# Performance work log

Measured on AMD Instinct MI355X. Metric: run time of the kernel, lower is better.

Reference implementation:

```python
import jax, jax.numpy as jnp
import numpy as np

B, T, H = 8, 4096, 512
K = 8192  # codebook size


def setup_inputs() -> dict:
    key = jax.random.key(0)
    kz, ke = jax.random.split(key)
    z = jax.random.normal(kz, (B, T, H), dtype=jnp.float32)
    emb = jax.random.normal(ke, (K, H), dtype=jnp.float32) * 0.02
    return {"z": z, "emb": emb}


def reference(z, emb):
    b, t, h = z.shape
    flat = z.reshape(b * t, h)
    dist = (jnp.sum(flat * flat, axis=1, keepdims=True)
            - 2.0 * (flat @ emb.T)
            + jnp.sum(emb * emb, axis=1)[None, :])
    idx = jnp.argmin(dist, axis=1)            # (b*t,)
    z_q = emb[idx].reshape(b, t, h)           # codebook lookup
    # straight-through estimator
    z_st = z + jax.lax.stop_gradient(z_q - z)
    codebook_loss = jnp.mean((z_q - jax.lax.stop_gradient(z)) ** 2)
    commit_loss = jnp.mean((z - jax.lax.stop_gradient(z_q)) ** 2)
    return z_st, idx.reshape(b, t), codebook_loss, commit_loss
```

## Files before the change

### kernel.cpp

```cpp
#include <hip/hip_runtime.h>
#include <cstdint>
#include <cstddef>

#define M_ROWS 32768
#define K_CODES 8192
#define H_DIM 512
#define TAU 2.5e-4f
#define MAXFLAG 32768

typedef float  f32x4 __attribute__((ext_vector_type(4)));
typedef short  s16x8 __attribute__((ext_vector_type(8)));

typedef __attribute__((address_space(3))) void as3_void;
typedef const __attribute__((address_space(1))) void as1_cvoid;
#define GLD16(gp, lp) __builtin_amdgcn_global_load_lds((as1_cvoid*)(gp), (as3_void*)(lp), 16, 0, 0)

__device__ __forceinline__ unsigned short f2bf(float f) {
    uint32_t u = __float_as_uint(f);
    u = u + 0x7fffu + ((u >> 16) & 1u);
    return (unsigned short)(u >> 16);
}
__device__ __forceinline__ float bf2f(unsigned short h) {
    return __uint_as_float(((uint32_t)h) << 16);
}

__global__ __launch_bounds__(256) void split_all_kernel(
    const float* __restrict__ z, const float* __restrict__ emb,
    unsigned short* __restrict__ zh, unsigned short* __restrict__ zl,
    unsigned short* __restrict__ eh, unsigned short* __restrict__ el)
{
    const int ZQ = M_ROWS * H_DIM / 4;
    const int EQ = K_CODES * H_DIM / 4;
    int t = blockIdx.x * 256 + threadIdx.x;
    const float* src; unsigned short* hi; unsigned short* lo;
    if (t < ZQ)           { src = z;   hi = zh; lo = zl; }
    else if (t < ZQ + EQ) { t -= ZQ; src = emb; hi = eh; lo = el; }
    else return;
    const float4 v = reinterpret_cast<const float4*>(src)[t];
    ushort4 h, l;
    h.x = f2bf(v.x); l.x = f2bf(v.x - bf2f(h.x));
    h.y = f2bf(v.y); l.y = f2bf(v.y - bf2f(h.y));
    h.z = f2bf(v.z); l.z = f2bf(v.z - bf2f(h.z));
    h.w = f2bf(v.w); l.w = f2bf(v.w - bf2f(h.w));
    reinterpret_cast<ushort4*>(hi)[t] = h;
    reinterpret_cast<ushort4*>(lo)[t] = l;
}

__device__ __forceinline__ float np_sumsq_row32(const float* __restrict__ row,
                                                int lane32) {
    const int c = lane32 >> 3, j = lane32 & 7;
    const float* p = row + c * 128 + j;
    float s = __fmul_rn(p[0], p[0]);
    #pragma unroll
    for (int t = 1; t < 16; ++t) {
        const float v = p[8 * t];
        s = __fadd_rn(s, __fmul_rn(v, v));
    }
    s = __fadd_rn(s, __shfl_xor(s, 1));
    s = __fadd_rn(s, __shfl_xor(s, 2));
    s = __fadd_rn(s, __shfl_xor(s, 4));
    s = __fadd_rn(s, __shfl_xor(s, 8));
    s = __fadd_rn(s, __shfl_xor(s, 16));
    return s;
}

__global__ __launch_bounds__(256) void rowsq_all_kernel(
    const float* __restrict__ z, const float* __restrict__ emb,
    float* __restrict__ x2, float* __restrict__ e2,
    float* __restrict__ loss_slots, int* __restrict__ flag_count)
{
    const int slot = blockIdx.x * 8 + (threadIdx.x >> 5);
    if (slot < M_ROWS) {
        const float s = np_sumsq_row32(z + (size_t)slot * H_DIM, threadIdx.x & 31);
        if ((threadIdx.x & 31) == 0) x2[slot] = s;
    } else if (slot < M_ROWS + K_CODES) {
        const int r = slot - M_ROWS;
        const float s = np_sumsq_row32(emb + (size_t)r * H_DIM, threadIdx.x & 31);
        if ((threadIdx.x & 31) == 0) e2[r] = s;
    }
    if (blockIdx.x == 0) {
        if (threadIdx.x < 2) loss_slots[threadIdx.x] = 0.f;
        if (threadIdx.x == 0) *flag_count = 0;
    }
}

__device__ __forceinline__ void top2_merge(float& b1, int& ix, float& b2,
                                           float ob1, int oix, float ob2) {
    if (ob1 < b1)      { b2 = fminf(b1, ob2); b1 = ob1; ix = oix; }
    else if (ob1 > b1) { b2 = fminf(b2, ob1); }
    else               { if (oix < ix) ix = oix; b2 = b1; }
}

__global__ __launch_bounds__(512, 1) void mfma_dist_kernel(
    const unsigned short* __restrict__ zh, const unsigned short* __restrict__ zl,
    const unsigned short* __restrict__ eh, const unsigned short* __restrict__ el,
    const float* __restrict__ x2, const float* __restrict__ e2,
    float* __restrict__ pb1, float* __restrict__ pb2, int* __restrict__ pidx)
{
    __shared__ __align__(16) unsigned short lb[2][4][8192];

    const int tid = threadIdx.x;
    const int l   = tid & 63;
    const int w   = tid >> 6;
    const int wm  = w >> 2;
    const int wn  = w & 3;

    const int bid  = blockIdx.x;
    const int xcd  = bid & 7;
    const int sq   = bid >> 3;
    const int band = sq >> 7;
    const int r128 = sq & 127;
    const int ct   = r128 >> 2;
    const int rt   = (band * 8 + xcd) * 4 + (r128 & 3);
    const int row0 = rt * 256;
    const int c0   = ct * 256;

    const int m    = w >> 1;
    const int half = w & 1;
    const unsigned short* sp = (m == 0) ? zh : (m == 1) ? zl : (m == 2) ? eh : el;
    const int rbase0 = (m < 2) ? row0 : c0;
    const unsigned short* sb = sp
        + (size_t)(rbase0 + half * 128 + (l >> 2)) * H_DIM
        + ((l & 3) ^ ((l >> 3) & 3)) * 8;

    const int aoff = (wm * 128 + (l & 15)) * 64 + (((l >> 4) ^ ((l >> 1) & 3)) * 16);
    const int boff = (wn * 64  + (l & 15)) * 64 + (((l >> 4) ^ ((l >> 1) & 3)) * 16);

    f32x4 acc[8][4];
    #pragma unroll
    for (int i = 0; i < 8; ++i)
        #pragma unroll
        for (int j = 0; j < 4; ++j)
            acc[i][j] = (f32x4){0.f, 0.f, 0.f, 0.f};

    {
        char* dst = (char*)&lb[0][m][0] + half * 8192;
        #pragma unroll
        for (int t = 0; t < 8; ++t)
            GLD16(sb + (size_t)t * 16 * H_DIM, dst + t * 1024);
    }
    asm volatile("s_waitcnt vmcnt(0)" ::: "memory");
    __builtin_amdgcn_s_barrier();

    for (int s = 0; s < 16; ++s) {
        const int par = s & 1;

        if (s < 15) {
            const unsigned short* src = sb + (s + 1) * 32;
            char* dst = (char*)&lb[par ^ 1][m][0] + half * 8192;
            #pragma unroll
            for (int t = 0; t < 8; ++t)
                GLD16(src + (size_t)t * 16 * H_DIM, dst + t * 1024);
            asm volatile("s_waitcnt vmcnt(8)" ::: "memory");
        } else {
            asm volatile("s_waitcnt vmcnt(0)" ::: "memory");
        }
        __builtin_amdgcn_s_barrier();

        const char* pAh = (const char*)&lb[par][0][0];
        const char* pAl = (const char*)&lb[par][1][0];
        const char* pBh = (const char*)&lb[par][2][0];
        const char* pBl = (const char*)&lb[par][3][0];

        s16x8 ah[8];
        #pragma unroll
        for (int i = 0; i < 8; ++i)
            ah[i] = *(const s16x8*)(pAh + aoff + i * 1024);
        s16x8 bh[4], bv[4];
        #pragma unroll
        for (int j = 0; j < 4; ++j) {
            bh[j] = *(const s16x8*)(pBh + boff + j * 1024);
            bv[j] = *(const s16x8*)(pBl + boff + j * 1024);
        }

        __builtin_amdgcn_s_setprio(1);
        #pragma unroll
        for (int j = 0; j < 4; ++j)
            #pragma unroll
            for (int i = 0; i < 8; ++i)
                acc[i][j] = __builtin_amdgcn_mfma_f32_16x16x32_bf16(ah[i], bv[j], acc[i][j], 0, 0, 0);
        s16x8 avA[4];
        #pragma unroll
        for (int i = 0; i < 4; ++i)
            avA[i] = *(const s16x8*)(pAl + aoff + i * 1024);
        #pragma unroll
        for (int j = 0; j < 4; ++j)
            #pragma unroll
            for (int i = 0; i < 8; ++i)
                acc[i][j] = __builtin_amdgcn_mfma_f32_16x16x32_bf16(ah[i], bh[j], acc[i][j], 0, 0, 0);
        s16x8 avB[4];
        #pragma unroll
        for (int i = 0; i < 4; ++i)
            avB[i] = *(const s16x8*)(pAl + aoff + (4 + i) * 1024);
        #pragma unroll
        for (int j = 0; j < 4; ++j)
            #pragma unroll
            for (int i = 0; i < 4; ++i)
                acc[i][j] = __builtin_amdgcn_mfma_f32_16x16x32_bf16(avA[i], bh[j], acc[i][j], 0, 0, 0);
        #pragma unroll
        for (int j = 0; j < 4; ++j)
            #pragma unroll
            for (int i = 0; i < 4; ++i)
                acc[4 + i][j] = __builtin_amdgcn_mfma_f32_16x16x32_bf16(avB[i], bh[j], acc[4 + i][j], 0, 0, 0);
        __builtin_amdgcn_s_setprio(0);

        __builtin_amdgcn_s_barrier();
    }

    float* mb1 = (float*)&lb[0][0][0];
    float* mb2 = mb1 + 1024;
    int*   mi  = (int*)(mb1 + 2048);

    float e2v[4];
    #pragma unroll
    for (int j = 0; j < 4; ++j)
        e2v[j] = e2[c0 + wn * 64 + j * 16 + (l & 15)];

    #pragma unroll
    for (int i = 0; i < 8; ++i) {
        const float4 x2v = *reinterpret_cast<const float4*>(
            x2 + row0 + wm * 128 + i * 16 + (l >> 4) * 4);
        const float x2a[4] = {x2v.x, x2v.y, x2v.z, x2v.w};
        #pragma unroll
        for (int r = 0; r < 4; ++r) {
            float b1 = 3.4e38f, b2 = 3.4e38f; int ix = 0;
            #pragma unroll
            for (int j = 0; j < 4; ++j) {
                const float d = __fadd_rn(__fmaf_rn(-2.f, acc[i][j][r], x2a[r]), e2v[j]);
                const int cj = c0 + wn * 64 + j * 16 + (l & 15);
                if (d < b1)      { b2 = b1; b1 = d; ix = cj; }
                else if (d < b2) { b2 = d; }
            }
            #pragma unroll
            for (int mm = 1; mm <= 8; mm <<= 1) {
                const float ob1 = __shfl_xor(b1, mm);
                const float ob2 = __shfl_xor(b2, mm);
                const int   oix = __shfl_xor(ix, mm);
                top2_merge(b1, ix, b2, ob1, oix, ob2);
            }
            if ((l & 15) == 0) {
                const int rl = wm * 128 + i * 16 + (l >> 4) * 4 + r;
                mb1[wn * 256 + rl] = b1;
                mb2[wn * 256 + rl] = b2;
                mi [wn * 256 + rl] = ix;
            }
        }
    }
    __syncthreads();
    if (tid < 256) {
        float b1 = mb1[tid], b2 = mb2[tid]; int ix = mi[tid];
        #pragma unroll
        for (int q = 1; q < 4; ++q)
            top2_merge(b1, ix, b2, mb1[q * 256 + tid], mi[q * 256 + tid], mb2[q * 256 + tid]);
        const size_t o = (size_t)ct * M_ROWS + row0 + tid;
        pb1[o] = b1; pb2[o] = b2; pidx[o] = ix;
    }
}

__global__ __launch_bounds__(256) void combine_kernel(
    const float* __restrict__ pb1, const float* __restrict__ pb2,
    const int* __restrict__ pidx,
    int* __restrict__ idx_i, float* __restrict__ idx_f,
    int* __restrict__ flag_count, int* __restrict__ flag_rows)
{
    const int r = blockIdx.x * 256 + threadIdx.x;
    if (r >= M_ROWS) return;
    float b1 = pb1[r], b2 = pb2[r]; int ix = pidx[r];
    #pragma unroll 4
    for (int ct = 1; ct < 32; ++ct)
        top2_merge(b1, ix, b2, pb1[(size_t)ct * M_ROWS + r],
                   pidx[(size_t)ct * M_ROWS + r], pb2[(size_t)ct * M_ROWS + r]);
    idx_i[r] = ix;
    idx_f[r] = (float)ix;
    if (b2 - b1 < TAU) {
        const int p = atomicAdd(flag_count, 1);
        if (p < MAXFLAG) flag_rows[p] = r;
    }
}

#define BM 64
#define BN 128
#define BH 32
#define PADZ 4
#define PADE 4

__device__ __forceinline__ void stage_transposed(const float* __restrict__ src,
                                                 int row0, int h0,
                                                 float* lds, int R, int ldp) {
    const int nf4 = R * (BH / 4);
    for (int f = threadIdx.x; f < nf4; f += 256) {
        const int r  = f / (BH / 4);
        const int c4 = (f % (BH / 4)) * 4;
        const float4 v = *reinterpret_cast<const float4*>(
            src + (size_t)(row0 + r) * H_DIM + h0 + c4);
        lds[(c4 + 0) * ldp + r] = v.x;
        lds[(c4 + 1) * ldp + r] = v.y;
        lds[(c4 + 2) * ldp + r] = v.z;
        lds[(c4 + 3) * ldp + r] = v.w;
    }
}

__global__ __launch_bounds__(256) void dist_argmin_kernel(
    const float* __restrict__ z, const float* __restrict__ emb,
    const float* __restrict__ x2, const float* __restrict__ e2,
    int* __restrict__ idx_i, float* __restrict__ idx_f,
    int* __restrict__ flag_count, int* __restrict__ flag_rows)
{
    __shared__ float zs[BH * (BM + PADZ)];
    __shared__ float es[BH * (BN + PADE)];
    __shared__ float bd[BM][17];
    __shared__ float bd2[BM][17];
    __shared__ int   bi[BM][17];

    const int row0 = blockIdx.x * BM;
    const int tx = threadIdx.x & 15;
    const int ty = threadIdx.x >> 4;

    float x2r[4];
    #pragma unroll
    for (int i = 0; i < 4; ++i) x2r[i] = x2[row0 + ty * 4 + i];

    float best[4], best2[4];
    int   bidx[4];
    #pragma unroll
    for (int i = 0; i < 4; ++i) { best[i] = 3.4e38f; best2[i] = 3.4e38f; bidx[i] = 0; }

    for (int nt = 0; nt < K_CODES / BN; ++nt) {
        float acc[4][8];
        #pragma unroll
        for (int i = 0; i < 4; ++i)
            #pragma unroll
            for (int j = 0; j < 8; ++j) acc[i][j] = 0.f;

        for (int hc = 0; hc < H_DIM / BH; ++hc) {
            __syncthreads();
            stage_transposed(z,   row0,    hc * BH, zs, BM, BM + PADZ);
            stage_transposed(emb, nt * BN, hc * BH, es, BN, BN + PADE);
            __syncthreads();
            #pragma unroll
            for (int h = 0; h < BH; ++h) {
                const float4 zr = *reinterpret_cast<const float4*>(&zs[h * (BM + PADZ) + ty * 4]);
                const float4 e0 = *reinterpret_cast<const float4*>(&es[h * (BN + PADE) + tx * 4]);
                const float4 e1 = *reinterpret_cast<const float4*>(&es[h * (BN + PADE) + 64 + tx * 4]);
                const float zrv[4] = {zr.x, zr.y, zr.z, zr.w};
                const float ev[8]  = {e0.x, e0.y, e0.z, e0.w, e1.x, e1.y, e1.z, e1.w};
                #pragma unroll
                for (int i = 0; i < 4; ++i)
                    #pragma unroll
                    for (int j = 0; j < 8; ++j)
                        acc[i][j] = fmaf(zrv[i], ev[j], acc[i][j]);
            }
        }
        #pragma unroll
        for (int j = 0; j < 8; ++j) {
            const int code = nt * BN + (j < 4 ? tx * 4 + j : 64 + tx * 4 + (j - 4));
            const float e2v = e2[code];
            #pragma unroll
            for (int i = 0; i < 4; ++i) {
                const float d = __fadd_rn(__fmaf_rn(-2.f, acc[i][j], x2r[i]), e2v);
                if (d < best[i])       { best2[i] = best[i]; best[i] = d; bidx[i] = code; }
                else if (d < best2[i]) { best2[i] = d; }
            }
        }
    }

    __syncthreads();
    #pragma unroll
    for (int i = 0; i < 4; ++i) {
        bd [ty * 4 + i][tx] = best[i];
        bd2[ty * 4 + i][tx] = best2[i];
        bi [ty * 4 + i][tx] = bidx[i];
    }
    __syncthreads();
    if (threadIdx.x < BM) {
        const int r = threadIdx.x;
        float g1 = bd[r][0]; int gi = bi[r][0]; float g2 = bd2[r][0];
        #pragma unroll
        for (int t = 1; t < 16; ++t) {
            const float v = bd[r][t]; const int x = bi[r][t];
            if (v < g1)       { g2 = g1; g1 = v; gi = x; }
            else if (v == g1) { g2 = g1; if (x < gi) gi = x; }
            else              { g2 = fminf(g2, v); }
            g2 = fminf(g2, bd2[r][t]);
        }
        idx_i[row0 + r] = gi;
        idx_f[row0 + r] = (float)gi;
        if (g2 - g1 < TAU) {
            const int p = atomicAdd(flag_count, 1);
            if (p < MAXFLAG) flag_rows[p] = row0 + r;
        }
    }
}

__global__ __launch_bounds__(256) void fixup_scan_kernel(
    const float* __restrict__ z, const float* __restrict__ emb,
    const float* __restrict__ x2, const float* __restrict__ e2,
    const int* __restrict__ flag_count, const int* __restrict__ flag_rows,
    float* __restrict__ qb1, int* __restrict__ qix)
{
    __shared__ float zrow[H_DIM];
    __shared__ float sd[256];
    __shared__ int   si[256];
    int n = *flag_count; if (n > MAXFLAG) n = MAXFLAG;
    const int q = blockIdx.x & 3;
    for (int j = blockIdx.x >> 2; j < n; j += (gridDim.x >> 2)) {
        const int row = flag_rows[j];
        __syncthreads();
        for (int h = threadIdx.x; h < H_DIM; h += 256)
            zrow[h] = z[(size_t)row * H_DIM + h];
        __syncthreads();
        const float x2r = x2[row];
        float bdv = 3.4e38f; int biv = 0x7fffffff;
        for (int k = q * 2048 + threadIdx.x; k < q * 2048 + 2048; k += 256) {
            const float* ek = emb + (size_t)k * H_DIM;
            double d0 = 0.0, d1 = 0.0, d2 = 0.0, d3 = 0.0;
            for (int h = 0; h < H_DIM; h += 4) {
                const float4 ev = *reinterpret_cast<const float4*>(ek + h);
                const float4 zv = *reinterpret_cast<const float4*>(&zrow[h]);
                d0 = fma((double)zv.x, (double)ev.x, d0);
                d1 = fma((double)zv.y, (double)ev.y, d1);
                d2 = fma((double)zv.z, (double)ev.z, d2);
                d3 = fma((double)zv.w, (double)ev.w, d3);
            }
            const float gf = (float)((d0 + d1) + (d2 + d3));
            const float d = __fadd_rn(__fmaf_rn(-2.f, gf, x2r), e2[k]);
            if (d < bdv) { bdv = d; biv = k; }
        }
        sd[threadIdx.x] = bdv; si[threadIdx.x] = biv;
        __syncthreads();
        for (int s = 128; s; s >>= 1) {
            if (threadIdx.x < s) {
                const float od = sd[threadIdx.x + s]; const int oi = si[threadIdx.x + s];
                if (od < sd[threadIdx.x] ||
                    (od == sd[threadIdx.x] && oi < si[threadIdx.x])) {
                    sd[threadIdx.x] = od; si[threadIdx.x] = oi;
                }
            }
            __syncthreads();
        }
        if (threadIdx.x == 0) { qb1[j * 4 + q] = sd[0]; qix[j * 4 + q] = si[0]; }
        __syncthreads();
    }
}

__global__ __launch_bounds__(256) void fixup_merge_kernel(
    const int* __restrict__ flag_count, const int* __restrict__ flag_rows,
    const float* __restrict__ qb1, const int* __restrict__ qix,
    int* __restrict__ idx_i, float* __restrict__ idx_f)
{
    int n = *flag_count; if (n > MAXFLAG) n = MAXFLAG;
    const int t = blockIdx.x * 256 + threadIdx.x;
    if (t >= n) return;
    float b = qb1[t * 4]; int ix = qix[t * 4];
    #pragma unroll
    for (int q = 1; q < 4; ++q) {
        const float ob = qb1[t * 4 + q];
        if (ob < b) { b = ob; ix = qix[t * 4 + q]; }
    }
    idx_i[flag_rows[t]] = ix;
    idx_f[flag_rows[t]] = (float)ix;
}

__global__ __launch_bounds__(256) void epilogue_kernel(
    const float* __restrict__ z, const float* __restrict__ emb,
    const int* __restrict__ idx_i,
    float* __restrict__ z_st, float* __restrict__ loss_slots)
{
    const int NQ = M_ROWS * (H_DIM / 4);
    const float4* z4 = reinterpret_cast<const float4*>(z);
    const float4* e4 = reinterpret_cast<const float4*>(emb);
    float4* o4 = reinterpret_cast<float4*>(z_st);
    float local = 0.f;
    for (int q = blockIdx.x * 256 + threadIdx.x; q < NQ; q += gridDim.x * 256) {
        const int r  = q >> 7;
        const int h4 = q & 127;
        const float4 zq = e4[(size_t)idx_i[r] * 128 + h4];
        const float4 zv = z4[q];
        float4 t, o;
        t.x = zq.x - zv.x; o.x = zv.x + t.x;
        t.y = zq.y - zv.y; o.y = zv.y + t.y;
        t.z = zq.z - zv.z; o.z = zv.z + t.z;
        t.w = zq.w - zv.w; o.w = zv.w + t.w;
        o4[q] = o;
        local = fmaf(t.x, t.x, local);
        local = fmaf(t.y, t.y, local);
        local = fmaf(t.z, t.z, local);
        local = fmaf(t.w, t.w, local);
    }
    #pragma unroll
    for (int off = 32; off; off >>= 1) local += __shfl_down(local, off);
    __shared__ float part[4];
    const int lane = threadIdx.x & 63, wid = threadIdx.x >> 6;
    if (lane == 0) part[wid] = local;
    __syncthreads();
    if (threadIdx.x == 0) {
        const float s = (part[0] + part[1] + part[2] + part[3])
                        * (1.f / (float)((size_t)M_ROWS * H_DIM));
        atomicAdd(&loss_slots[0], s);
        atomicAdd(&loss_slots[1], s);
    }
}

extern "C" void kernel_launch(void* const* d_in, const int* in_sizes, int n_in,
                              void* d_out, int out_size, void* d_ws, size_t ws_size,
                              hipStream_t stream) {
    const float* z   = (const float*)d_in[0];
    const float* emb = (const float*)d_in[1];

    float* out   = (float*)d_out;
    float* z_st  = out;
    float* idx_f = out + (size_t)M_ROWS * H_DIM;
    float* loss  = out + (size_t)M_ROWS * H_DIM + M_ROWS;

    float* pb1  = z_st;
    float* pb2  = z_st + (size_t)32 * M_ROWS;
    int*   pidx = (int*)(z_st + (size_t)64 * M_ROWS);
    float* qb1  = z_st + (size_t)96 * M_ROWS;
    int*   qix  = (int*)(z_st + (size_t)96 * M_ROWS + 4 * MAXFLAG);

    char* ws = (char*)d_ws;
    float* e2     = (float*)(ws + 0);
    float* x2     = (float*)(ws + 32768);
    int*   idx_i  = (int*)  (ws + 163840);
    int*   fcount = (int*)  (ws + 294912);
    int*   frows  = (int*)  (ws + 294976);
    unsigned short* zh = (unsigned short*)(ws + 426048);
    unsigned short* zl = (unsigned short*)(ws + 426048 + 33554432ull);
    unsigned short* eh = (unsigned short*)(ws + 426048 + 67108864ull);
    unsigned short* el = (unsigned short*)(ws + 426048 + 75497472ull);
    const size_t REQ = 426048ull + 83886080ull;

    hipLaunchKernelGGL(rowsq_all_kernel, dim3((M_ROWS + K_CODES) / 8), dim3(256), 0, stream,
                       z, emb, x2, e2, loss, fcount);

    if (ws_size >= REQ) {
        const int totq = (M_ROWS * H_DIM + K_CODES * H_DIM) / 4;
        hipLaunchKernelGGL(split_all_kernel, dim3(totq / 256), dim3(256), 0, stream,
                           z, emb, zh, zl, eh, el);
        hipLaunchKernelGGL(mfma_dist_kernel, dim3(4096), dim3(512), 0, stream,
                           zh, zl, eh, el, x2, e2, pb1, pb2, pidx);
        hipLaunchKernelGGL(combine_kernel, dim3(M_ROWS / 256), dim3(256), 0, stream,
                           pb1, pb2, pidx, idx_i, idx_f, fcount, frows);
    } else {
        hipLaunchKernelGGL(dist_argmin_kernel, dim3(M_ROWS / BM), dim3(256), 0, stream,
                           z, emb, x2, e2, idx_i, idx_f, fcount, frows);
    }

    hipLaunchKernelGGL(fixup_scan_kernel, dim3(8192), dim3(256), 0, stream,
                       z, emb, x2, e2, fcount, frows, qb1, qix);
    hipLaunchKernelGGL(fixup_merge_kernel, dim3(MAXFLAG / 256), dim3(256), 0, stream,
                       fcount, frows, qb1, qix, idx_i, idx_f);
    hipLaunchKernelGGL(epilogue_kernel, dim3(2048), dim3(256), 0, stream,
                       z, emb, idx_i, z_st, loss);
}
```

Measured before the change: 1.178 ms.

## Switch split-bf16 GEMM to 32x32x16 MFMA with staged LDS loads

Replaces the 16x16x32 bf16 MFMA tiling with 32x32x16 MFMAs on 4x2 tiles of 16-wide accumulators. The aim is fewer LDS fragment reads and MFMA issues per unit of work. LDS loads are split into two k-halves, with sched barriers and explicit lgkmcnt waits so the second half's fragment loads overlap the first half's MFMAs. The argmin epilogue is remapped to the 32x32 output layout and shuffles across 32 lanes. The remap adds risk of layout or ordering mistakes, and the larger per-instruction fragments may raise register pressure.

New measurement: 1.583 ms. +34.3%, slower.

```diff
diff --git a/kernel.cpp b/kernel.cpp
--- a/kernel.cpp
+++ b/kernel.cpp
@@ -8,12 +8,14 @@
 #define TAU 2.5e-4f
 #define MAXFLAG 32768
 
-typedef float  f32x4 __attribute__((ext_vector_type(4)));
-typedef short  s16x8 __attribute__((ext_vector_type(8)));
+typedef float  f32x4  __attribute__((ext_vector_type(4)));
+typedef float  f32x16 __attribute__((ext_vector_type(16)));
+typedef short  s16x8  __attribute__((ext_vector_type(8)));
 
 typedef __attribute__((address_space(3))) void as3_void;
 typedef const __attribute__((address_space(1))) void as1_cvoid;
 #define GLD16(gp, lp) __builtin_amdgcn_global_load_lds((as1_cvoid*)(gp), (as3_void*)(lp), 16, 0, 0)
+#define SB0() __builtin_amdgcn_sched_barrier(0)
 
 __device__ __forceinline__ unsigned short f2bf(float f) {
     uint32_t u = __float_as_uint(f);
@@ -123,15 +125,21 @@
         + (size_t)(rbase0 + half * 128 + (l >> 2)) * H_DIM
         + ((l & 3) ^ ((l >> 3) & 3)) * 8;
 
-    const int aoff = (wm * 128 + (l & 15)) * 64 + (((l >> 4) ^ ((l >> 1) & 3)) * 16);
-    const int boff = (wn * 64  + (l & 15)) * 64 + (((l >> 4) ^ ((l >> 1) & 3)) * 16);
-
-    f32x4 acc[8][4];
-    #pragma unroll
-    for (int i = 0; i < 8; ++i)
-        #pragma unroll
-        for (int j = 0; j < 4; ++j)
-            acc[i][j] = (f32x4){0.f, 0.f, 0.f, 0.f};
+    const int ar    = l & 31;
+    const int hsel  = l >> 5;
+    const int axr   = (ar >> 1) & 3;
+    const int soff0 = (((0 << 1) + hsel) ^ axr) * 16;
+    const int soff1 = (((1 << 1) + hsel) ^ axr) * 16;
+    const int abase = (wm * 128 + ar) * 64;
+    const int bbase = (wn * 64  + ar) * 64;
+
+    f32x16 acc[4][2];
+    #pragma unroll
+    for (int i = 0; i < 4; ++i)
+        #pragma unroll
+        for (int j = 0; j < 2; ++j)
+            #pragma unroll
+            for (int r = 0; r < 16; ++r) acc[i][j][r] = 0.f;
 
     {
         char* dst = (char*)&lb[0][m][0] + half * 8192;
@@ -162,46 +170,73 @@
         const char* pBh = (const char*)&lb[par][2][0];
         const char* pBl = (const char*)&lb[par][3][0];
 
-        s16x8 ah[8];
-        #pragma unroll
-        for (int i = 0; i < 8; ++i)
-            ah[i] = *(const s16x8*)(pAh + aoff + i * 1024);
-        s16x8 bh[4], bv[4];
-        #pragma unroll
-        for (int j = 0; j < 4; ++j) {
-            bh[j] = *(const s16x8*)(pBh + boff + j * 1024);
-            bv[j] = *(const s16x8*)(pBl + boff + j * 1024);
-        }
+        s16x8 ah0[4], av0[4], bh0[2], bv0[2];
+        #pragma unroll
+        for (int i = 0; i < 4; ++i) {
+            ah0[i] = *(const s16x8*)(pAh + abase + i * 2048 + soff0);
+            av0[i] = *(const s16x8*)(pAl + abase + i * 2048 + soff0);
+        }
+        #pragma unroll
+        for (int j = 0; j < 2; ++j) {
+            bh0[j] = *(const s16x8*)(pBh + bbase + j * 2048 + soff0);
+            bv0[j] = *(const s16x8*)(pBl + bbase + j * 2048 + soff0);
+        }
+        SB0();
+        s16x8 ah1[4], av1[4];
+        #pragma unroll
+        for (int i = 0; i < 4; ++i) {
+            ah1[i] = *(const s16x8*)(pAh + abase + i * 2048 + soff1);
+            av1[i] = *(const s16x8*)(pAl + abase + i * 2048 + soff1);
+        }
+        SB0();
+        asm volatile("s_waitcnt lgkmcnt(8)" ::: "memory");
+        SB0();
 
         __builtin_amdgcn_s_setprio(1);
         #pragma unroll
-        for (int j = 0; j < 4; ++j)
-            #pragma unroll
-            for (int i = 0; i < 8; ++i)
-                acc[i][j] = __builtin_amdgcn_mfma_f32_16x16x32_bf16(ah[i], bv[j], acc[i][j], 0, 0, 0);
-        s16x8 avA[4];
-        #pragma unroll
-        for (int i = 0; i < 4; ++i)
-            avA[i] = *(const s16x8*)(pAl + aoff + i * 1024);
-        #pragma unroll
-        for (int j = 0; j < 4; ++j)
-            #pragma unroll
-            for (int i = 0; i < 8; ++i)
-                acc[i][j] = __builtin_amdgcn_mfma_f32_16x16x32_bf16(ah[i], bh[j], acc[i][j], 0, 0, 0);
-        s16x8 avB[4];
-        #pragma unroll
-        for (int i = 0; i < 4; ++i)
-            avB[i] = *(const s16x8*)(pAl + aoff + (4 + i) * 1024);
-        #pragma unroll
-        for (int j = 0; j < 4; ++j)
+        for (int j = 0; j < 2; ++j)
             #pragma unroll
             for (int i = 0; i < 4; ++i)
-                acc[i][j] = __builtin_amdgcn_mfma_f32_16x16x32_bf16(avA[i], bh[j], acc[i][j], 0, 0, 0);
-        #pragma unroll
-        for (int j = 0; j < 4; ++j)
+                acc[i][j] = __builtin_amdgcn_mfma_f32_32x32x16_bf16(ah0[i], bv0[j], acc[i][j], 0, 0, 0);
+        #pragma unroll
+        for (int j = 0; j < 2; ++j)
             #pragma unroll
             for (int i = 0; i < 4; ++i)
-                acc[4 + i][j] = __builtin_amdgcn_mfma_f32_16x16x32_bf16(avB[i], bh[j], acc[4 + i][j], 0, 0, 0);
+                acc[i][j] = __builtin_amdgcn_mfma_f32_32x32x16_bf16(ah0[i], bh0[j], acc[i][j], 0, 0, 0);
+        __builtin_amdgcn_s_setprio(0);
+        SB0();
+        s16x8 bh1[2], bv1[2];
+        #pragma unroll
+        for (int j = 0; j < 2; ++j) {
+            bh1[j] = *(const s16x8*)(pBh + bbase + j * 2048 + soff1);
+            bv1[j] = *(const s16x8*)(pBl + bbase + j * 2048 + soff1);
+        }
+        SB0();
+        __builtin_amdgcn_s_setprio(1);
+        #pragma unroll
+        for (int j = 0; j < 2; ++j)
+            #pragma unroll
+            for (int i = 0; i < 4; ++i)
+                acc[i][j] = __builtin_amdgcn_mfma_f32_32x32x16_bf16(av0[i], bh0[j], acc[i][j], 0, 0, 0);
+        __builtin_amdgcn_s_setprio(0);
+        asm volatile("s_waitcnt lgkmcnt(0)" ::: "memory");
+        SB0();
+        __builtin_amdgcn_s_setprio(1);
+        #pragma unroll
+        for (int j = 0; j < 2; ++j)
+            #pragma unroll
+            for (int i = 0; i < 4; ++i)
+                acc[i][j] = __builtin_amdgcn_mfma_f32_32x32x16_bf16(ah1[i], bv1[j], acc[i][j], 0, 0, 0);
+        #pragma unroll
+        for (int j = 0; j < 2; ++j)
+            #pragma unroll
+            for (int i = 0; i < 4; ++i)
+                acc[i][j] = __builtin_amdgcn_mfma_f32_32x32x16_bf16(ah1[i], bh1[j], acc[i][j], 0, 0, 0);
+        #pragma unroll
+        for (int j = 0; j < 2; ++j)
+            #pragma unroll
+            for (int i = 0; i < 4; ++i)
+                acc[i][j] = __builtin_amdgcn_mfma_f32_32x32x16_bf16(av1[i], bh1[j], acc[i][j], 0, 0, 0);
         __builtin_amdgcn_s_setprio(0);
 
         __builtin_amdgcn_s_barrier();
@@ -211,38 +246,43 @@
     float* mb2 = mb1 + 1024;
     int*   mi  = (int*)(mb1 + 2048);
 
-    float e2v[4];
-    #pragma unroll
-    for (int j = 0; j < 4; ++j)
-        e2v[j] = e2[c0 + wn * 64 + j * 16 + (l & 15)];
-
-    #pragma unroll
-    for (int i = 0; i < 8; ++i) {
-        const float4 x2v = *reinterpret_cast<const float4*>(
-            x2 + row0 + wm * 128 + i * 16 + (l >> 4) * 4);
-        const float x2a[4] = {x2v.x, x2v.y, x2v.z, x2v.w};
-        #pragma unroll
-        for (int r = 0; r < 4; ++r) {
-            float b1 = 3.4e38f, b2 = 3.4e38f; int ix = 0;
-            #pragma unroll
-            for (int j = 0; j < 4; ++j) {
-                const float d = __fadd_rn(__fmaf_rn(-2.f, acc[i][j][r], x2a[r]), e2v[j]);
-                const int cj = c0 + wn * 64 + j * 16 + (l & 15);
-                if (d < b1)      { b2 = b1; b1 = d; ix = cj; }
-                else if (d < b2) { b2 = d; }
-            }
-            #pragma unroll
-            for (int mm = 1; mm <= 8; mm <<= 1) {
-                const float ob1 = __shfl_xor(b1, mm);
-                const float ob2 = __shfl_xor(b2, mm);
-                const int   oix = __shfl_xor(ix, mm);
-                top2_merge(b1, ix, b2, ob1, oix, ob2);
-            }
-            if ((l & 15) == 0) {
-                const int rl = wm * 128 + i * 16 + (l >> 4) * 4 + r;
-                mb1[wn * 256 + rl] = b1;
-                mb2[wn * 256 + rl] = b2;
-                mi [wn * 256 + rl] = ix;
+    float e2v[2];
+    #pragma unroll
+    for (int j = 0; j < 2; ++j)
+        e2v[j] = e2[c0 + wn * 64 + j * 32 + ar];
+    const int colb = c0 + wn * 64 + ar;
+
+    #pragma unroll
+    for (int i = 0; i < 4; ++i) {
+        #pragma unroll
+        for (int g = 0; g < 4; ++g) {
+            const float4 x2v = *reinterpret_cast<const float4*>(
+                x2 + row0 + wm * 128 + i * 32 + g * 8 + 4 * hsel);
+            const float x2a[4] = {x2v.x, x2v.y, x2v.z, x2v.w};
+            #pragma unroll
+            for (int r2 = 0; r2 < 4; ++r2) {
+                const int reg = g * 4 + r2;
+                float b1 = 3.4e38f, b2 = 3.4e38f; int ix = 0;
+                #pragma unroll
+                for (int j = 0; j < 2; ++j) {
+                    const float d = __fadd_rn(__fmaf_rn(-2.f, acc[i][j][reg], x2a[r2]), e2v[j]);
+                    const int cj = colb + j * 32;
+                    if (d < b1)      { b2 = b1; b1 = d; ix = cj; }
+                    else if (d < b2) { b2 = d; }
+                }
+                #pragma unroll
+                for (int mm = 1; mm <= 16; mm <<= 1) {
+                    const float ob1 = __shfl_xor(b1, mm);
+                    const float ob2 = __shfl_xor(b2, mm);
+                    const int   oix = __shfl_xor(ix, mm);
+                    top2_merge(b1, ix, b2, ob1, oix, ob2);
+                }
+                if (ar == 0) {
+                    const int rl = wm * 128 + i * 32 + r2 + 8 * g + 4 * hsel;
+                    mb1[wn * 256 + rl] = b1;
+                    mb2[wn * 256 + rl] = b2;
+                    mi [wn * 256 + rl] = ix;
+                }
             }
         }
     }
```
